# Optimization experiments

Measured on AMD Instinct MI355X. Metric: run time of the kernel, lower is better.

## Reference

```python
import jax, jax.numpy as jnp
import numpy as np
import math

B, T, C, H, E = 1, 384, 512, 8, 16
D = C // H

def layer_norm(x, w, b, eps=1e-5):
    mu = jnp.mean(x, axis=-1, keepdims=True)
    var = jnp.mean(jnp.square(x - mu), axis=-1, keepdims=True)
    return (x - mu) * jax.lax.rsqrt(var + eps) * w + b

def setup_inputs() -> dict:
    key = jax.random.key(0)
    ks = jax.random.split(key, 12)
    s = 0.02
    return {
        'x': jax.random.normal(ks[0], (B, T, C), jnp.float32),
        'bias_matrix': jax.random.randint(ks[1], (B, T, T), 0, E, jnp.int32),
        'ln1_w': jnp.ones((C,), jnp.float32),
        'ln1_b': jnp.zeros((C,), jnp.float32),
        'w_attn_w': jax.random.normal(ks[2], (3 * C, C), jnp.float32) * s,
        'w_attn_b': jnp.zeros((3 * C,), jnp.float32),
        'w_proj_w': jax.random.normal(ks[3], (C, C), jnp.float32) * s,
        'w_proj_b': jnp.zeros((C,), jnp.float32),
        'attn_bias_emb': jax.random.normal(ks[4], (E, H), jnp.float32) * s,
        'edge_emb': jax.random.normal(ks[5], (E, C), jnp.float32) * s,
        'w_edge_k_w': jax.random.normal(ks[6], (C, C), jnp.float32) * s,
        'w_edge_k_b': jnp.zeros((C,), jnp.float32),
        'w_edge_v_w': jax.random.normal(ks[7], (C, C), jnp.float32) * s,
        'w_edge_v_b': jnp.zeros((C,), jnp.float32),
        'ln2_w': jnp.ones((C,), jnp.float32),
        'ln2_b': jnp.zeros((C,), jnp.float32),
        'c_fc_w': jax.random.normal(ks[8], (4 * C, C), jnp.float32) * s,
        'c_fc_b': jnp.zeros((4 * C,), jnp.float32),
        'c_proj_w': jax.random.normal(ks[9], (C, 4 * C), jnp.float32) * s,
        'c_proj_b': jnp.zeros((C,), jnp.float32),
    }

def reference(x, bias_matrix, ln1_w, ln1_b, w_attn_w, w_attn_b, w_proj_w, w_proj_b,
              attn_bias_emb, edge_emb, w_edge_k_w, w_edge_k_b, w_edge_v_w, w_edge_v_b,
              ln2_w, ln2_b, c_fc_w, c_fc_b, c_proj_w, c_proj_b):
    # --- attention branch ---
    h = layer_norm(x, ln1_w, ln1_b)
    qkv = h @ w_attn_w.T + w_attn_b                      # (B,T,3C)
    q, k, v = jnp.split(qkv, 3, axis=-1)
    q = q.reshape(B, T, H, D).transpose(0, 2, 1, 3)      # (B,H,T,D)
    k = k.reshape(B, T, H, D).transpose(0, 2, 1, 3)
    v = v.reshape(B, T, H, D).transpose(0, 2, 1, 3)
    scale = math.sqrt(D)

    ee = edge_emb[bias_matrix]                           # (B,T,T,C)
    e_k = (ee @ w_edge_k_w.T + w_edge_k_b).reshape(B, T, T, H, D)
    # score[b,h,i,j] = sum_d q[b,h,i,d] * k[b,h,j,d] * e_k[b,i,j,h,d]
    scores = jnp.einsum('bhid,bhjd,bijhd->bhij', q, k, e_k) / scale

    mask = jnp.tril(jnp.ones((T, T), bool))              # causal, diag included
    scores = jnp.where(mask, scores, -jnp.inf)
    ab = attn_bias_emb[bias_matrix].transpose(0, 3, 1, 2)  # (B,H,T,T)
    ab = jnp.where(mask, ab, 0.0)
    attn = jax.nn.softmax(scores + ab, axis=-1)

    e_v = (ee @ w_edge_v_w.T + w_edge_v_b).reshape(B, T, T, H, D)
    # y[b,h,i,d] = sum_j attn[b,h,i,j] * v[b,h,j,d] * e_v[b,i,j,h,d]
    y = jnp.einsum('bhij,bhjd,bijhd->bhid', attn, v, e_v)
    y = y.transpose(0, 2, 1, 3).reshape(B, T, C)
    y = y @ w_proj_w.T + w_proj_b
    x = x + y

    # --- MLP branch ---
    h2 = layer_norm(x, ln2_w, ln2_b)
    h2 = jax.nn.gelu(h2 @ c_fc_w.T + c_fc_b, approximate=False)
    x = x + (h2 @ c_proj_w.T + c_proj_b)
    return x
```

## Files before the change

kernel.cpp:

```cpp
#include <hip/hip_runtime.h>
#include <math.h>

#define TT 384
#define CC 512
#define HH 8
#define EE 16

typedef __bf16 bf16_t;
typedef __bf16 bf16x8 __attribute__((ext_vector_type(8)));
typedef __bf16 bf16x4v __attribute__((ext_vector_type(4)));
typedef float f32x4 __attribute__((ext_vector_type(4)));

__device__ __forceinline__ float wave_reduce_sum(float v) {
#pragma unroll
  for (int off = 32; off >= 1; off >>= 1) v += __shfl_xor(v, off, 64);
  return v;
}

__device__ __forceinline__ void wrow_unit(const float* __restrict__ wr,
                                          const float* __restrict__ g,
                                          const float* __restrict__ bb,
                                          float extra_c, bf16_t* __restrict__ orow,
                                          float* __restrict__ s1p,
                                          float* __restrict__ cp, int lane) {
  const float* p = wr + lane * 8;
  f32x4 w0 = *(const f32x4*)p, w1 = *(const f32x4*)(p + 4);
  f32x4 g0 = *(const f32x4*)(g + lane * 8), g1 = *(const f32x4*)(g + lane * 8 + 4);
  f32x4 b0 = *(const f32x4*)(bb + lane * 8), b1 = *(const f32x4*)(bb + lane * 8 + 4);
  f32x4 p0 = w0 * g0, p1 = w1 * g1;
  bf16x8 o;
  o[0] = (bf16_t)p0.x; o[1] = (bf16_t)p0.y; o[2] = (bf16_t)p0.z; o[3] = (bf16_t)p0.w;
  o[4] = (bf16_t)p1.x; o[5] = (bf16_t)p1.y; o[6] = (bf16_t)p1.z; o[7] = (bf16_t)p1.w;
  *(bf16x8*)(orow + lane * 8) = o;
  float s1 = p0.x + p0.y + p0.z + p0.w + p1.x + p1.y + p1.z + p1.w;
  float c = w0.x * b0.x + w0.y * b0.y + w0.z * b0.z + w0.w * b0.w +
            w1.x * b1.x + w1.y * b1.y + w1.z * b1.z + w1.w * b1.w;
  s1 = wave_reduce_sum(s1);
  c = wave_reduce_sum(c);
  if (lane == 0) { *s1p = s1; *cp = c + extra_c; }
}

struct PrepX {
  const float *eemb, *wekw, *wekb, *wevw, *wevb;
  const float *ln2w, *ln2b, *cfcw, *cfcb;
  const float *wproj, *wcproj;
  float *ektab, *evtab, *s1f, *cf, *x1s1, *x1s2;
  bf16_t *wfc_bf, *wproj_bf, *wcproj_bf;
};

__device__ void prep_unit(int u, const PrepX& X, int tid) {
  int lane = tid & 63, wave = tid >> 6;
  if (u < 256) {
    int wid = u * 4 + wave;
    int gbase = wid * 16;
    int table = gbase >> 13;
    int e = (gbase >> 9) & 15;
    int c0 = gbase & 511;
    const float* er = X.eemb + e * 512 + lane * 8;
    f32x4 ea = *(const f32x4*)er;
    f32x4 eb = *(const f32x4*)(er + 4);
    const float* wbase = table ? X.wevw : X.wekw;
    const float* bbase = table ? X.wevb : X.wekb;
    float* obase = (table ? X.evtab : X.ektab) + e * 512;
#pragma unroll
    for (int o = 0; o < 16; o++) {
      int c = c0 + o;
      const float* wr = wbase + (size_t)c * 512 + lane * 8;
      f32x4 wa = *(const f32x4*)wr;
      f32x4 wb = *(const f32x4*)(wr + 4);
      float acc = ea.x * wa.x + ea.y * wa.y + ea.z * wa.z + ea.w * wa.w +
                  eb.x * wb.x + eb.y * wb.y + eb.z * wb.z + eb.w * wb.w;
      acc = wave_reduce_sum(acc);
      if (lane == 0) obase[c] = acc + bbase[c];
    }
  } else if (u < 768) {
    int n = (u - 256) * 4 + wave;
    wrow_unit(X.cfcw + (size_t)n * 512, X.ln2w, X.ln2b, X.cfcb[n],
              X.wfc_bf + (size_t)n * 512, X.s1f + n, X.cf + n, lane);
  } else if (u < 1024) {
    int base = (u - 768) * 1024;
    for (int t = tid; t < 1024; t += 256) {
      f32x4 a = *((const f32x4*)X.wcproj + base + t);
      bf16x4v o;
      o[0] = (bf16_t)a.x; o[1] = (bf16_t)a.y; o[2] = (bf16_t)a.z; o[3] = (bf16_t)a.w;
      *((bf16x4v*)X.wcproj_bf + base + t) = o;
    }
  } else if (u < 1088) {
    int base = (u - 1024) * 1024;
    for (int t = tid; t < 1024; t += 256) {
      f32x4 a = *((const f32x4*)X.wproj + base + t);
      bf16x4v o;
      o[0] = (bf16_t)a.x; o[1] = (bf16_t)a.y; o[2] = (bf16_t)a.z; o[3] = (bf16_t)a.w;
      *((bf16x4v*)X.wproj_bf + base + t) = o;
    }
  } else if (u == 1088) {
    for (int i = tid; i < 384; i += 256) { X.x1s1[i] = 0.f; X.x1s2[i] = 0.f; }
  }
}

__global__ __launch_bounds__(256) void qkv_k(
    const float* __restrict__ x, const float* __restrict__ wattn,
    const float* __restrict__ ln1w, const float* __restrict__ ln1b,
    const float* __restrict__ wattnb, bf16_t* __restrict__ out, PrepX X) {
  int tid = threadIdx.x;
  if (blockIdx.y >= 12) {
    prep_unit((blockIdx.y - 12) * gridDim.x + blockIdx.x, X, tid);
    return;
  }
  __shared__ float part[4][32][32];
  __shared__ float rst[2][4][32];
  __shared__ float wst[2][4][32];
  int lane = tid & 63, wave = tid >> 6;
  int m0 = blockIdx.y * 32, n0 = blockIdx.x * 32;
  int r16 = lane & 15, quad = lane >> 4;
  int k0 = wave * 128;

  f32x4 acc[2][2];
  f32x4 zero = {0.f, 0.f, 0.f, 0.f};
#pragma unroll
  for (int i = 0; i < 2; i++)
#pragma unroll
    for (int j = 0; j < 2; j++) acc[i][j] = zero;

  const float* Af = x + (size_t)(m0 + r16) * 512 + k0 + quad * 8;
  const float* Wf = wattn + (size_t)(n0 + r16) * 512 + k0 + quad * 8;
  const float* gp = ln1w + k0 + quad * 8;
  const float* bp = ln1b + k0 + quad * 8;

  float sx[2] = {0.f, 0.f}, sxx[2] = {0.f, 0.f};
  float s1[2] = {0.f, 0.f}, cc[2] = {0.f, 0.f};

  for (int kb0 = 0; kb0 < 128; kb0 += 64) {
    uint4 araw[2][2][2], wraw[2][2][2];
#pragma unroll
    for (int u = 0; u < 2; u++) {
      int kb = kb0 + u * 32;
#pragma unroll
      for (int t = 0; t < 2; t++) {
        araw[u][t][0] = *(const uint4*)(Af + (size_t)t * 16 * 512 + kb);
        araw[u][t][1] = *(const uint4*)(Af + (size_t)t * 16 * 512 + kb + 4);
        wraw[u][t][0] = *(const uint4*)(Wf + (size_t)t * 16 * 512 + kb);
        wraw[u][t][1] = *(const uint4*)(Wf + (size_t)t * 16 * 512 + kb + 4);
      }
    }
#pragma unroll
    for (int u = 0; u < 2; u++) {
      int kb = kb0 + u * 32;
      f32x4 g0 = *(const f32x4*)(gp + kb), g1 = *(const f32x4*)(gp + kb + 4);
      f32x4 b0 = *(const f32x4*)(bp + kb), b1 = *(const f32x4*)(bp + kb + 4);
      bf16x8 af[2], bfr[2];
#pragma unroll
      for (int t = 0; t < 2; t++) {
        f32x4 a0 = *reinterpret_cast<const f32x4*>(&araw[u][t][0]);
        f32x4 a1 = *reinterpret_cast<const f32x4*>(&araw[u][t][1]);
        af[t][0] = (bf16_t)a0.x; af[t][1] = (bf16_t)a0.y;
        af[t][2] = (bf16_t)a0.z; af[t][3] = (bf16_t)a0.w;
        af[t][4] = (bf16_t)a1.x; af[t][5] = (bf16_t)a1.y;
        af[t][6] = (bf16_t)a1.z; af[t][7] = (bf16_t)a1.w;
        sx[t] += a0.x + a0.y + a0.z + a0.w + a1.x + a1.y + a1.z + a1.w;
        sxx[t] += a0.x * a0.x + a0.y * a0.y + a0.z * a0.z + a0.w * a0.w +
                  a1.x * a1.x + a1.y * a1.y + a1.z * a1.z + a1.w * a1.w;
        f32x4 w0 = *reinterpret_cast<const f32x4*>(&wraw[u][t][0]);
        f32x4 w1 = *reinterpret_cast<const f32x4*>(&wraw[u][t][1]);
        f32x4 p0 = w0 * g0, p1 = w1 * g1;
        bfr[t][0] = (bf16_t)p0.x; bfr[t][1] = (bf16_t)p0.y;
        bfr[t][2] = (bf16_t)p0.z; bfr[t][3] = (bf16_t)p0.w;
        bfr[t][4] = (bf16_t)p1.x; bfr[t][5] = (bf16_t)p1.y;
        bfr[t][6] = (bf16_t)p1.z; bfr[t][7] = (bf16_t)p1.w;
        s1[t] += p0.x + p0.y + p0.z + p0.w + p1.x + p1.y + p1.z + p1.w;
        cc[t] += w0.x * b0.x + w0.y * b0.y + w0.z * b0.z + w0.w * b0.w +
                 w1.x * b1.x + w1.y * b1.y + w1.z * b1.z + w1.w * b1.w;
      }
#pragma unroll
      for (int i = 0; i < 2; i++)
#pragma unroll
        for (int j = 0; j < 2; j++)
          acc[i][j] = __builtin_amdgcn_mfma_f32_16x16x32_bf16(af[i], bfr[j],
                                                              acc[i][j], 0, 0, 0);
    }
  }

#pragma unroll
  for (int t = 0; t < 2; t++) {
    sx[t] += __shfl_xor(sx[t], 16, 64);  sx[t] += __shfl_xor(sx[t], 32, 64);
    sxx[t] += __shfl_xor(sxx[t], 16, 64); sxx[t] += __shfl_xor(sxx[t], 32, 64);
    s1[t] += __shfl_xor(s1[t], 16, 64);  s1[t] += __shfl_xor(s1[t], 32, 64);
    cc[t] += __shfl_xor(cc[t], 16, 64);  cc[t] += __shfl_xor(cc[t], 32, 64);
  }
  if (quad == 0) {
#pragma unroll
    for (int t = 0; t < 2; t++) {
      rst[0][wave][t * 16 + r16] = sx[t];
      rst[1][wave][t * 16 + r16] = sxx[t];
      wst[0][wave][t * 16 + r16] = s1[t];
      wst[1][wave][t * 16 + r16] = cc[t];
    }
  }
#pragma unroll
  for (int i = 0; i < 2; i++)
#pragma unroll
    for (int j = 0; j < 2; j++)
#pragma unroll
      for (int r = 0; r < 4; r++)
        part[wave][i * 16 + quad * 4 + r][j * 16 + r16] = acc[i][j][r];
  __syncthreads();

  int row = tid >> 3, c4 = (tid & 7) * 4;
  f32x4 v = *(const f32x4*)&part[0][row][c4];
  v += *(const f32x4*)&part[1][row][c4];
  v += *(const f32x4*)&part[2][row][c4];
  v += *(const f32x4*)&part[3][row][c4];
  float sxt = rst[0][0][row] + rst[0][1][row] + rst[0][2][row] + rst[0][3][row];
  float sxxt = rst[1][0][row] + rst[1][1][row] + rst[1][2][row] + rst[1][3][row];
  float mu = sxt * (1.0f / 512.0f);
  float var = sxxt * (1.0f / 512.0f) - mu * mu;
  float rs = rsqrtf(var + 1e-5f);
  int grow = m0 + row, gcol = n0 + c4;
  bf16x4v o;
#pragma unroll
  for (int t = 0; t < 4; t++) {
    int cl = c4 + t;
    float s1v = wst[0][0][cl] + wst[0][1][cl] + wst[0][2][cl] + wst[0][3][cl];
    float ccv = wst[1][0][cl] + wst[1][1][cl] + wst[1][2][cl] + wst[1][3][cl] +
                wattnb[n0 + cl];
    o[t] = (bf16_t)(rs * (v[t] - mu * s1v) + ccv);
  }
  *(bf16x4v*)(out + (size_t)grow * 1536 + gcol) = o;
}

template <int MODE>
__global__ __launch_bounds__(256) void gemm_k(
    const void* __restrict__ Aptr, const bf16_t* __restrict__ Wb,
    const float* __restrict__ e0, const float* __restrict__ e1,
    const float* __restrict__ e2, const float* __restrict__ e3,
    const float* __restrict__ res, void* __restrict__ out,
    float* __restrict__ st1, float* __restrict__ st2, int N, int K) {
  constexpr bool AF32 = (MODE == 2);
  constexpr int AW = AF32 ? 2 : 1;
  __shared__ float part[4][32][32];
  int tid = threadIdx.x;
  int lane = tid & 63, wave = tid >> 6;
  int m0 = blockIdx.y * 32, n0 = blockIdx.x * 32;
  int r16 = lane & 15, quad = lane >> 4;
  int kchunk = K >> 2, k0 = wave * kchunk;

  f32x4 acc[2][2];
  f32x4 zero = {0.f, 0.f, 0.f, 0.f};
#pragma unroll
  for (int i = 0; i < 2; i++)
#pragma unroll
    for (int j = 0; j < 2; j++) acc[i][j] = zero;

  const float* Af = (const float*)Aptr + (size_t)(m0 + r16) * K + k0 + quad * 8;
  const bf16_t* Ab = (const bf16_t*)Aptr + (size_t)(m0 + r16) * K + k0 + quad * 8;
  const bf16_t* Wp = Wb + (size_t)(n0 + r16) * K + k0 + quad * 8;

  for (int kb0 = 0; kb0 < kchunk; kb0 += 128) {
    uint4 araw[4][2][AW];
    uint4 braw[4][2];
#pragma unroll
    for (int u = 0; u < 4; u++) {
      int kb = kb0 + u * 32;
#pragma unroll
      for (int t = 0; t < 2; t++) {
        if (AF32) {
          araw[u][t][0] = *(const uint4*)(Af + (size_t)t * 16 * K + kb);
          araw[u][t][1] = *(const uint4*)(Af + (size_t)t * 16 * K + kb + 4);
        } else {
          araw[u][t][0] = *(const uint4*)(Ab + (size_t)t * 16 * K + kb);
        }
        braw[u][t] = *(const uint4*)(Wp + (size_t)t * 16 * K + kb);
      }
    }
#pragma unroll
    for (int u = 0; u < 4; u++) {
      bf16x8 af[2], bfr[2];
#pragma unroll
      for (int t = 0; t < 2; t++) {
        if (AF32) {
          f32x4 a = *reinterpret_cast<const f32x4*>(&araw[u][t][0]);
          f32x4 c = *reinterpret_cast<const f32x4*>(&araw[u][t][1]);
          af[t][0] = (bf16_t)a.x; af[t][1] = (bf16_t)a.y;
          af[t][2] = (bf16_t)a.z; af[t][3] = (bf16_t)a.w;
          af[t][4] = (bf16_t)c.x; af[t][5] = (bf16_t)c.y;
          af[t][6] = (bf16_t)c.z; af[t][7] = (bf16_t)c.w;
        } else {
          af[t] = *reinterpret_cast<const bf16x8*>(&araw[u][t][0]);
        }
        bfr[t] = *reinterpret_cast<const bf16x8*>(&braw[u][t]);
      }
#pragma unroll
      for (int i = 0; i < 2; i++)
#pragma unroll
        for (int j = 0; j < 2; j++)
          acc[i][j] = __builtin_amdgcn_mfma_f32_16x16x32_bf16(af[i], bfr[j],
                                                              acc[i][j], 0, 0, 0);
    }
  }

#pragma unroll
  for (int i = 0; i < 2; i++)
#pragma unroll
    for (int j = 0; j < 2; j++)
#pragma unroll
      for (int r = 0; r < 4; r++)
        part[wave][i * 16 + quad * 4 + r][j * 16 + r16] = acc[i][j][r];
  __syncthreads();

  int row = tid >> 3, c4 = (tid & 7) * 4;
  f32x4 v = *(const f32x4*)&part[0][row][c4];
  v += *(const f32x4*)&part[1][row][c4];
  v += *(const f32x4*)&part[2][row][c4];
  v += *(const f32x4*)&part[3][row][c4];
  int grow = m0 + row, gcol = n0 + c4;

  if (MODE == 2) {
    float S = e0[grow], Q = e1[grow];
    float mu = S * (1.0f / 512.0f);
    float var = Q * (1.0f / 512.0f) - mu * mu;
    float rs = rsqrtf(var + 1e-5f);
    f32x4 s1v = *(const f32x4*)(e2 + gcol);
    f32x4 ccv = *(const f32x4*)(e3 + gcol);
    bf16x4v o;
#pragma unroll
    for (int t = 0; t < 4; t++) {
      float xg = rs * (v[t] - mu * s1v[t]) + ccv[t];
      xg = 0.5f * xg * (1.0f + erff(xg * 0.70710678118654752f));
      o[t] = (bf16_t)xg;
    }
    *(bf16x4v*)((bf16_t*)out + (size_t)grow * N + gcol) = o;
  } else {
    v += *(const f32x4*)(e2 + gcol);
    v += *(const f32x4*)(res + (size_t)grow * N + gcol);
    *(f32x4*)((float*)out + (size_t)grow * N + gcol) = v;
    if (MODE == 1) {
      float sv = v.x + v.y + v.z + v.w;
      float qv = v.x * v.x + v.y * v.y + v.z * v.z + v.w * v.w;
      sv += __shfl_down(sv, 4, 8); qv += __shfl_down(qv, 4, 8);
      sv += __shfl_down(sv, 2, 8); qv += __shfl_down(qv, 2, 8);
      sv += __shfl_down(sv, 1, 8); qv += __shfl_down(qv, 1, 8);
      if ((tid & 7) == 0) {
        atomicAdd(st1 + grow, sv);
        atomicAdd(st2 + grow, qv);
      }
    }
  }
}

__global__ __launch_bounds__(256) void attn_k(
    const bf16_t* __restrict__ qkv, const int* __restrict__ bias_matrix,
    const float* __restrict__ attn_bias_emb, const float* __restrict__ ek_tab,
    const float* __restrict__ ev_tab, bf16_t* __restrict__ ybuf) {
  __shared__ int ebuf[TT];
  __shared__ uint2 ps[TT];
  __shared__ float qe[EE][68];
  __shared__ float evh[EE * 64];
  __shared__ float red[4 * 64];
  __shared__ float absh[EE];
  __shared__ float scr[4];

  int i = (TT - 1) - blockIdx.x, h = blockIdx.y;
  int tid = threadIdx.x, lane = tid & 63, wave = tid >> 6;
  int n = i + 1;

  for (int j = tid; j < n; j += 256) ebuf[j] = bias_matrix[i * TT + j];
  if (tid < EE) absh[tid] = attn_bias_emb[tid * HH + h];
  for (int idx = tid; idx < EE * 64; idx += 256) {
    int e = idx >> 6, d = idx & 63;
    float qv = (float)qkv[(size_t)i * 1536 + h * 64 + d];
    qe[e][d] = qv * ek_tab[e * 512 + h * 64 + d];
    evh[idx] = ev_tab[e * 512 + h * 64 + d];
  }
  __syncthreads();

  float ls = 0.0f;
  for (int jl = tid; jl < n; jl += 256) {
    int e = ebuf[jl];
    const uint4* kp = (const uint4*)(qkv + (size_t)jl * 1536 + 512 + h * 64);
    uint4 kr[8];
#pragma unroll
    for (int dg = 0; dg < 8; dg++) kr[dg] = kp[dg];
    float acc = 0.f;
#pragma unroll
    for (int dg = 0; dg < 8; dg++) {
      bf16x8 kv = *reinterpret_cast<const bf16x8*>(&kr[dg]);
      f32x4 qa = *(const f32x4*)&qe[e][dg * 8];
      f32x4 qb = *(const f32x4*)&qe[e][dg * 8 + 4];
      acc += (float)kv[0] * qa.x + (float)kv[1] * qa.y + (float)kv[2] * qa.z +
             (float)kv[3] * qa.w + (float)kv[4] * qb.x + (float)kv[5] * qb.y +
             (float)kv[6] * qb.z + (float)kv[7] * qb.w;
    }
    float p = __expf(acc * 0.125f + absh[e]);
    uint2 pk;
    pk.x = (unsigned)e;
    pk.y = __float_as_uint(p);
    ps[jl] = pk;
    ls += p;
  }
  ls = wave_reduce_sum(ls);
  if (lane == 0) scr[wave] = ls;
  __syncthreads();
  float inv = 1.0f / (scr[0] + scr[1] + scr[2] + scr[3]);

  const bf16_t* vb = qkv + 1024 + h * 64 + lane;
  float acc = 0.0f;
  int j = wave;
  for (; j + 12 < n; j += 16) {
    uint2 a0 = ps[j];
    uint2 a1 = ps[j + 4];
    uint2 a2 = ps[j + 8];
    uint2 a3 = ps[j + 12];
    float v0 = (float)vb[(size_t)j * 1536];
    float v1 = (float)vb[(size_t)(j + 4) * 1536];
    float v2 = (float)vb[(size_t)(j + 8) * 1536];
    float v3 = (float)vb[(size_t)(j + 12) * 1536];
    float e0 = evh[a0.x * 64 + lane];
    float e1 = evh[a1.x * 64 + lane];
    float e2 = evh[a2.x * 64 + lane];
    float e3 = evh[a3.x * 64 + lane];
    acc = fmaf(__uint_as_float(a0.y) * v0, e0, acc);
    acc = fmaf(__uint_as_float(a1.y) * v1, e1, acc);
    acc = fmaf(__uint_as_float(a2.y) * v2, e2, acc);
    acc = fmaf(__uint_as_float(a3.y) * v3, e3, acc);
  }
  for (; j < n; j += 4) {
    uint2 a0 = ps[j];
    float v0 = (float)vb[(size_t)j * 1536];
    acc = fmaf(__uint_as_float(a0.y) * v0, evh[a0.x * 64 + lane], acc);
  }
  red[wave * 64 + lane] = acc;
  __syncthreads();
  if (tid < 64) {
    float y = (red[tid] + red[64 + tid] + red[128 + tid] + red[192 + tid]) * inv;
    ybuf[(size_t)i * CC + h * 64 + tid] = (bf16_t)y;
  }
}

extern "C" void kernel_launch(void* const* d_in, const int* in_sizes, int n_in,
                              void* d_out, int out_size, void* d_ws,
                              size_t ws_size, hipStream_t stream) {
  const float* x = (const float*)d_in[0];
  const int* bias_mat = (const int*)d_in[1];

  char* wp = (char*)d_ws;
  float* ektab = (float*)wp;  wp += 16 * 512 * 4;
  float* evtab = (float*)wp;  wp += 16 * 512 * 4;
  float* x1s1 = (float*)wp;   wp += 384 * 4;
  float* x1s2 = (float*)wp;   wp += 384 * 4;
  float* s1f = (float*)wp;    wp += 2048 * 4;
  float* cf = (float*)wp;     wp += 2048 * 4;
  float* x1 = (float*)wp;     wp += 384 * 512 * 4;
  bf16_t* wfc_bf = (bf16_t*)wp;    wp += 2048 * 512 * 2;
  bf16_t* wproj_bf = (bf16_t*)wp;  wp += 512 * 512 * 2;
  bf16_t* wcproj_bf = (bf16_t*)wp; wp += 512 * 2048 * 2;
  bf16_t* qkv = (bf16_t*)wp;  wp += 384 * 1536 * 2;
  bf16_t* ybuf = (bf16_t*)wp; wp += 384 * 512 * 2;
  bf16_t* gbuf = (bf16_t*)wp; wp += 384 * 2048 * 2;

  PrepX X;
  X.eemb = (const float*)d_in[9];
  X.wekw = (const float*)d_in[10];
  X.wekb = (const float*)d_in[11];
  X.wevw = (const float*)d_in[12];
  X.wevb = (const float*)d_in[13];
  X.ln2w = (const float*)d_in[14];
  X.ln2b = (const float*)d_in[15];
  X.cfcw = (const float*)d_in[16];
  X.cfcb = (const float*)d_in[17];
  X.wproj = (const float*)d_in[6];
  X.wcproj = (const float*)d_in[18];
  X.ektab = ektab; X.evtab = evtab; X.s1f = s1f; X.cf = cf;
  X.x1s1 = x1s1; X.x1s2 = x1s2;
  X.wfc_bf = wfc_bf; X.wproj_bf = wproj_bf; X.wcproj_bf = wcproj_bf;

  qkv_k<<<dim3(48, 35), 256, 0, stream>>>(
      x, (const float*)d_in[4], (const float*)d_in[2], (const float*)d_in[3],
      (const float*)d_in[5], qkv, X);
  attn_k<<<dim3(TT, HH), 256, 0, stream>>>(qkv, bias_mat,
                                           (const float*)d_in[8], ektab, evtab,
                                           ybuf);
  gemm_k<1><<<dim3(16, 12), 256, 0, stream>>>(
      ybuf, wproj_bf, nullptr, nullptr, (const float*)d_in[7], nullptr, x, x1,
      x1s1, x1s2, 512, 512);
  gemm_k<2><<<dim3(64, 12), 256, 0, stream>>>(x1, wfc_bf, x1s1, x1s2, s1f, cf,
                                              nullptr, gbuf, nullptr, nullptr,
                                              2048, 512);
  gemm_k<3><<<dim3(16, 12), 256, 0, stream>>>(
      gbuf, wcproj_bf, nullptr, nullptr, (const float*)d_in[19], nullptr, x1,
      d_out, nullptr, nullptr, 512, 2048);
}
```

Baseline: 173.8 us.

## Batch four balanced query rows per attention block and compute LN2 stats in-GEMM

The attention kernel now processes four query rows per block, paired (i, 383-i, and two middle rows) so causal work is balanced across blocks. K and V loads are shared across the four rows, cutting global traffic and launching a quarter as many blocks. Separately, the LayerNorm-2 row statistics are now computed inside the fc GEMM from its fp32 A loads, rather than by atomics in the projection epilogue. This removes the atomics and the zero-init work, but uses more shared memory and registers per attention block, which may reduce occupancy.

```diff
diff --git a/kernel.cpp b/kernel.cpp
--- a/kernel.cpp
+++ b/kernel.cpp
@@ -44,7 +44,7 @@
   const float *eemb, *wekw, *wekb, *wevw, *wevb;
   const float *ln2w, *ln2b, *cfcw, *cfcb;
   const float *wproj, *wcproj;
-  float *ektab, *evtab, *s1f, *cf, *x1s1, *x1s2;
+  float *ektab, *evtab, *s1f, *cf;
   bf16_t *wfc_bf, *wproj_bf, *wcproj_bf;
 };
 
@@ -93,8 +93,6 @@
       o[0] = (bf16_t)a.x; o[1] = (bf16_t)a.y; o[2] = (bf16_t)a.z; o[3] = (bf16_t)a.w;
       *((bf16x4v*)X.wproj_bf + base + t) = o;
     }
-  } else if (u == 1088) {
-    for (int i = tid; i < 384; i += 256) { X.x1s1[i] = 0.f; X.x1s2[i] = 0.f; }
   }
 }
 
@@ -231,13 +229,12 @@
 template <int MODE>
 __global__ __launch_bounds__(256) void gemm_k(
     const void* __restrict__ Aptr, const bf16_t* __restrict__ Wb,
-    const float* __restrict__ e0, const float* __restrict__ e1,
     const float* __restrict__ e2, const float* __restrict__ e3,
-    const float* __restrict__ res, void* __restrict__ out,
-    float* __restrict__ st1, float* __restrict__ st2, int N, int K) {
+    const float* __restrict__ res, void* __restrict__ out, int N, int K) {
   constexpr bool AF32 = (MODE == 2);
   constexpr int AW = AF32 ? 2 : 1;
   __shared__ float part[4][32][32];
+  __shared__ float rst[2][4][32];
   int tid = threadIdx.x;
   int lane = tid & 63, wave = tid >> 6;
   int m0 = blockIdx.y * 32, n0 = blockIdx.x * 32;
@@ -254,6 +251,8 @@
   const float* Af = (const float*)Aptr + (size_t)(m0 + r16) * K + k0 + quad * 8;
   const bf16_t* Ab = (const bf16_t*)Aptr + (size_t)(m0 + r16) * K + k0 + quad * 8;
   const bf16_t* Wp = Wb + (size_t)(n0 + r16) * K + k0 + quad * 8;
+
+  float sx[2] = {0.f, 0.f}, sxx[2] = {0.f, 0.f};
 
   for (int kb0 = 0; kb0 < kchunk; kb0 += 128) {
     uint4 araw[4][2][AW];
@@ -284,6 +283,9 @@
           af[t][2] = (bf16_t)a.z; af[t][3] = (bf16_t)a.w;
           af[t][4] = (bf16_t)c.x; af[t][5] = (bf16_t)c.y;
           af[t][6] = (bf16_t)c.z; af[t][7] = (bf16_t)c.w;
+          sx[t] += a.x + a.y + a.z + a.w + c.x + c.y + c.z + c.w;
+          sxx[t] += a.x * a.x + a.y * a.y + a.z * a.z + a.w * a.w +
+                    c.x * c.x + c.y * c.y + c.z * c.z + c.w * c.w;
         } else {
           af[t] = *reinterpret_cast<const bf16x8*>(&araw[u][t][0]);
         }
@@ -298,6 +300,20 @@
     }
   }
 
+  if (MODE == 2) {
+#pragma unroll
+    for (int t = 0; t < 2; t++) {
+      sx[t] += __shfl_xor(sx[t], 16, 64);  sx[t] += __shfl_xor(sx[t], 32, 64);
+      sxx[t] += __shfl_xor(sxx[t], 16, 64); sxx[t] += __shfl_xor(sxx[t], 32, 64);
+    }
+    if (quad == 0) {
+#pragma unroll
+      for (int t = 0; t < 2; t++) {
+        rst[0][wave][t * 16 + r16] = sx[t];
+        rst[1][wave][t * 16 + r16] = sxx[t];
+      }
+    }
+  }
 #pragma unroll
   for (int i = 0; i < 2; i++)
 #pragma unroll
@@ -315,7 +331,8 @@
   int grow = m0 + row, gcol = n0 + c4;
 
   if (MODE == 2) {
-    float S = e0[grow], Q = e1[grow];
+    float S = rst[0][0][row] + rst[0][1][row] + rst[0][2][row] + rst[0][3][row];
+    float Q = rst[1][0][row] + rst[1][1][row] + rst[1][2][row] + rst[1][3][row];
     float mu = S * (1.0f / 512.0f);
     float var = Q * (1.0f / 512.0f) - mu * mu;
     float rs = rsqrtf(var + 1e-5f);
@@ -333,16 +350,36 @@
     v += *(const f32x4*)(e2 + gcol);
     v += *(const f32x4*)(res + (size_t)grow * N + gcol);
     *(f32x4*)((float*)out + (size_t)grow * N + gcol) = v;
-    if (MODE == 1) {
-      float sv = v.x + v.y + v.z + v.w;
-      float qv = v.x * v.x + v.y * v.y + v.z * v.z + v.w * v.w;
-      sv += __shfl_down(sv, 4, 8); qv += __shfl_down(qv, 4, 8);
-      sv += __shfl_down(sv, 2, 8); qv += __shfl_down(qv, 2, 8);
-      sv += __shfl_down(sv, 1, 8); qv += __shfl_down(qv, 1, 8);
-      if ((tid & 7) == 0) {
-        atomicAdd(st1 + grow, sv);
-        atomicAdd(st2 + grow, qv);
-      }
+  }
+}
+
+template <int RC>
+__device__ __forceinline__ void pv_region(int& j, int jend,
+                                          const bf16_t* __restrict__ vb,
+                                          uint2 (*ps)[TT],
+                                          const float* __restrict__ evh,
+                                          int lane, float (&acc)[4]) {
+  for (; j + 12 < jend; j += 16) {
+    float v0 = (float)vb[(size_t)j * 1536];
+    float v1 = (float)vb[(size_t)(j + 4) * 1536];
+    float v2 = (float)vb[(size_t)(j + 8) * 1536];
+    float v3 = (float)vb[(size_t)(j + 12) * 1536];
+#pragma unroll
+    for (int r = 0; r < RC; r++) {
+      uint2 c0 = ps[r][j], c1 = ps[r][j + 4];
+      uint2 c2 = ps[r][j + 8], c3 = ps[r][j + 12];
+      acc[r] = fmaf(__uint_as_float(c0.y) * v0, evh[c0.x * 64 + lane], acc[r]);
+      acc[r] = fmaf(__uint_as_float(c1.y) * v1, evh[c1.x * 64 + lane], acc[r]);
+      acc[r] = fmaf(__uint_as_float(c2.y) * v2, evh[c2.x * 64 + lane], acc[r]);
+      acc[r] = fmaf(__uint_as_float(c3.y) * v3, evh[c3.x * 64 + lane], acc[r]);
+    }
+  }
+  for (; j < jend; j += 4) {
+    float v0 = (float)vb[(size_t)j * 1536];
+#pragma unroll
+    for (int r = 0; r < RC; r++) {
+      uint2 c0 = ps[r][j];
+      acc[r] = fmaf(__uint_as_float(c0.y) * v0, evh[c0.x * 64 + lane], acc[r]);
     }
   }
 }
@@ -351,88 +388,94 @@
     const bf16_t* __restrict__ qkv, const int* __restrict__ bias_matrix,
     const float* __restrict__ attn_bias_emb, const float* __restrict__ ek_tab,
     const float* __restrict__ ev_tab, bf16_t* __restrict__ ybuf) {
-  __shared__ int ebuf[TT];
-  __shared__ uint2 ps[TT];
-  __shared__ float qe[EE][68];
+  __shared__ uint2 ps[4][TT];
+  __shared__ float qe[4][EE][68];
   __shared__ float evh[EE * 64];
-  __shared__ float red[4 * 64];
+  __shared__ float red[4][256];
   __shared__ float absh[EE];
-  __shared__ float scr[4];
-
-  int i = (TT - 1) - blockIdx.x, h = blockIdx.y;
+  __shared__ float scr[4][4];
+
+  int b = blockIdx.x, h = blockIdx.y;
   int tid = threadIdx.x, lane = tid & 63, wave = tid >> 6;
-  int n = i + 1;
-
-  for (int j = tid; j < n; j += 256) ebuf[j] = bias_matrix[i * TT + j];
+  int rows[4] = {(TT - 1) - b, 192 + b, 191 - b, b};
+  int nn[4] = {TT - b, 193 + b, 192 - b, b + 1};
+
   if (tid < EE) absh[tid] = attn_bias_emb[tid * HH + h];
   for (int idx = tid; idx < EE * 64; idx += 256) {
     int e = idx >> 6, d = idx & 63;
-    float qv = (float)qkv[(size_t)i * 1536 + h * 64 + d];
-    qe[e][d] = qv * ek_tab[e * 512 + h * 64 + d];
+    float ek = ek_tab[e * 512 + h * 64 + d];
+#pragma unroll
+    for (int r = 0; r < 4; r++) {
+      float q = (float)qkv[(size_t)rows[r] * 1536 + h * 64 + d];
+      qe[r][e][d] = q * ek;
+    }
     evh[idx] = ev_tab[e * 512 + h * 64 + d];
   }
   __syncthreads();
 
-  float ls = 0.0f;
-  for (int jl = tid; jl < n; jl += 256) {
-    int e = ebuf[jl];
+  float ls[4] = {0.f, 0.f, 0.f, 0.f};
+  for (int jl = tid; jl < nn[0]; jl += 256) {
     const uint4* kp = (const uint4*)(qkv + (size_t)jl * 1536 + 512 + h * 64);
     uint4 kr[8];
 #pragma unroll
     for (int dg = 0; dg < 8; dg++) kr[dg] = kp[dg];
-    float acc = 0.f;
+    int ee[4];
+    float ac[4] = {0.f, 0.f, 0.f, 0.f};
+#pragma unroll
+    for (int r = 0; r < 4; r++)
+      ee[r] = (jl < nn[r]) ? bias_matrix[(size_t)rows[r] * TT + jl] : 0;
 #pragma unroll
     for (int dg = 0; dg < 8; dg++) {
       bf16x8 kv = *reinterpret_cast<const bf16x8*>(&kr[dg]);
-      f32x4 qa = *(const f32x4*)&qe[e][dg * 8];
-      f32x4 qb = *(const f32x4*)&qe[e][dg * 8 + 4];
-      acc += (float)kv[0] * qa.x + (float)kv[1] * qa.y + (float)kv[2] * qa.z +
-             (float)kv[3] * qa.w + (float)kv[4] * qb.x + (float)kv[5] * qb.y +
-             (float)kv[6] * qb.z + (float)kv[7] * qb.w;
-    }
-    float p = __expf(acc * 0.125f + absh[e]);
-    uint2 pk;
-    pk.x = (unsigned)e;
-    pk.y = __float_as_uint(p);
-    ps[jl] = pk;
-    ls += p;
-  }
-  ls = wave_reduce_sum(ls);
-  if (lane == 0) scr[wave] = ls;
+      float kf[8];
+#pragma unroll
+      for (int t = 0; t < 8; t++) kf[t] = (float)kv[t];
+#pragma unroll
+      for (int r = 0; r < 4; r++) {
+        f32x4 qa = *(const f32x4*)&qe[r][ee[r]][dg * 8];
+        f32x4 qb = *(const f32x4*)&qe[r][ee[r]][dg * 8 + 4];
+        ac[r] += kf[0] * qa.x + kf[1] * qa.y + kf[2] * qa.z + kf[3] * qa.w +
+                 kf[4] * qb.x + kf[5] * qb.y + kf[6] * qb.z + kf[7] * qb.w;
+      }
+    }
+#pragma unroll
+    for (int r = 0; r < 4; r++) {
+      if (jl < nn[r]) {
+        float p = __expf(ac[r] * 0.125f + absh[ee[r]]);
+        uint2 pk;
+        pk.x = (unsigned)ee[r];
+        pk.y = __float_as_uint(p);
+        ps[r][jl] = pk;
+        ls[r] += p;
+      }
+    }
+  }
+#pragma unroll
+  for (int r = 0; r < 4; r++) {
+    ls[r] = wave_reduce_sum(ls[r]);
+    if (lane == 0) scr[r][wave] = ls[r];
+  }
   __syncthreads();
-  float inv = 1.0f / (scr[0] + scr[1] + scr[2] + scr[3]);
 
   const bf16_t* vb = qkv + 1024 + h * 64 + lane;
-  float acc = 0.0f;
+  float acc[4] = {0.f, 0.f, 0.f, 0.f};
   int j = wave;
-  for (; j + 12 < n; j += 16) {
-    uint2 a0 = ps[j];
-    uint2 a1 = ps[j + 4];
-    uint2 a2 = ps[j + 8];
-    uint2 a3 = ps[j + 12];
-    float v0 = (float)vb[(size_t)j * 1536];
-    float v1 = (float)vb[(size_t)(j + 4) * 1536];
-    float v2 = (float)vb[(size_t)(j + 8) * 1536];
-    float v3 = (float)vb[(size_t)(j + 12) * 1536];
-    float e0 = evh[a0.x * 64 + lane];
-    float e1 = evh[a1.x * 64 + lane];
-    float e2 = evh[a2.x * 64 + lane];
-    float e3 = evh[a3.x * 64 + lane];
-    acc = fmaf(__uint_as_float(a0.y) * v0, e0, acc);
-    acc = fmaf(__uint_as_float(a1.y) * v1, e1, acc);
-    acc = fmaf(__uint_as_float(a2.y) * v2, e2, acc);
-    acc = fmaf(__uint_as_float(a3.y) * v3, e3, acc);
-  }
-  for (; j < n; j += 4) {
-    uint2 a0 = ps[j];
-    float v0 = (float)vb[(size_t)j * 1536];
-    acc = fmaf(__uint_as_float(a0.y) * v0, evh[a0.x * 64 + lane], acc);
-  }
-  red[wave * 64 + lane] = acc;
+  pv_region<4>(j, nn[3], vb, ps, evh, lane, acc);
+  pv_region<3>(j, nn[2], vb, ps, evh, lane, acc);
+  pv_region<2>(j, nn[1], vb, ps, evh, lane, acc);
+  pv_region<1>(j, nn[0], vb, ps, evh, lane, acc);
+#pragma unroll
+  for (int r = 0; r < 4; r++) red[r][wave * 64 + lane] = acc[r];
   __syncthreads();
-  if (tid < 64) {
-    float y = (red[tid] + red[64 + tid] + red[128 + tid] + red[192 + tid]) * inv;
-    ybuf[(size_t)i * CC + h * 64 + tid] = (bf16_t)y;
+
+  {
+    int r = tid >> 6, t = tid & 63;
+    int ir = (r == 0) ? (TT - 1 - b) : (r == 1) ? (192 + b)
+             : (r == 2) ? (191 - b) : b;
+    float iv = 1.0f / (scr[r][0] + scr[r][1] + scr[r][2] + scr[r][3]);
+    float y =
+        (red[r][t] + red[r][64 + t] + red[r][128 + t] + red[r][192 + t]) * iv;
+    ybuf[(size_t)ir * CC + h * 64 + t] = (bf16_t)y;
   }
 }
 
@@ -445,8 +488,6 @@
   char* wp = (char*)d_ws;
   float* ektab = (float*)wp;  wp += 16 * 512 * 4;
   float* evtab = (float*)wp;  wp += 16 * 512 * 4;
-  float* x1s1 = (float*)wp;   wp += 384 * 4;
-  float* x1s2 = (float*)wp;   wp += 384 * 4;
   float* s1f = (float*)wp;    wp += 2048 * 4;
   float* cf = (float*)wp;     wp += 2048 * 4;
   float* x1 = (float*)wp;     wp += 384 * 512 * 4;
@@ -470,22 +511,18 @@
   X.wproj = (const float*)d_in[6];
   X.wcproj = (const float*)d_in[18];
   X.ektab = ektab; X.evtab = evtab; X.s1f = s1f; X.cf = cf;
-  X.x1s1 = x1s1; X.x1s2 = x1s2;
   X.wfc_bf = wfc_bf; X.wproj_bf = wproj_bf; X.wcproj_bf = wcproj_bf;
 
   qkv_k<<<dim3(48, 35), 256, 0, stream>>>(
       x, (const float*)d_in[4], (const float*)d_in[2], (const float*)d_in[3],
       (const float*)d_in[5], qkv, X);
-  attn_k<<<dim3(TT, HH), 256, 0, stream>>>(qkv, bias_mat,
-                                           (const float*)d_in[8], ektab, evtab,
-                                           ybuf);
+  attn_k<<<dim3(TT / 4, HH), 256, 0, stream>>>(qkv, bias_mat,
+                                               (const float*)d_in[8], ektab,
+                                               evtab, ybuf);
   gemm_k<1><<<dim3(16, 12), 256, 0, stream>>>(
-      ybuf, wproj_bf, nullptr, nullptr, (const float*)d_in[7], nullptr, x, x1,
-      x1s1, x1s2, 512, 512);
-  gemm_k<2><<<dim3(64, 12), 256, 0, stream>>>(x1, wfc_bf, x1s1, x1s2, s1f, cf,
-                                              nullptr, gbuf, nullptr, nullptr,
-                                              2048, 512);
+      ybuf, wproj_bf, (const float*)d_in[7], nullptr, x, x1, 512, 512);
+  gemm_k<2><<<dim3(64, 12), 256, 0, stream>>>(x1, wfc_bf, s1f, cf, nullptr,
+                                              gbuf, 2048, 512);
   gemm_k<3><<<dim3(16, 12), 256, 0, stream>>>(
-      gbuf, wcproj_bf, nullptr, nullptr, (const float*)d_in[19], nullptr, x1,
-      d_out, nullptr, nullptr, 512, 2048);
-}
+      gbuf, wcproj_bf, (const float*)d_in[19], nullptr, x1, d_out, 512, 2048);
+}
```

Result: slower. 186.0 us (+7.0%).
